# Performance work log

Hardware: AMD Instinct MI355X
Metric: run time of the kernel (lower is better)

The kernel has to match this reference:

```python
import jax, jax.numpy as jnp
import numpy as np

D_IN = 1024
D_OUT = 1024
NUM_HEADS = 16
HEAD_DIM = D_OUT // NUM_HEADS


def setup_inputs() -> dict:
    key = jax.random.key(0)
    ks = jax.random.split(key, 6)
    scale = 0.02
    x = jax.random.normal(ks[0], (4, 2048, D_IN), dtype=jnp.float32)
    Wq = jax.random.normal(ks[1], (D_IN, D_OUT), dtype=jnp.float32) * scale
    Wk = jax.random.normal(ks[2], (D_IN, D_OUT), dtype=jnp.float32) * scale
    Wv = jax.random.normal(ks[3], (D_IN, D_OUT), dtype=jnp.float32) * scale
    Wo = jax.random.normal(ks[4], (D_OUT, D_OUT), dtype=jnp.float32) * scale
    bo = jax.random.normal(ks[5], (D_OUT,), dtype=jnp.float32) * scale
    return {"x": x, "Wq": Wq, "Wk": Wk, "Wv": Wv, "Wo": Wo, "bo": bo}


def reference(x, Wq, Wk, Wv, Wo, bo):
    b, n, _ = x.shape
    # QKV projections -> [b, h, n, hd]
    def split_heads(t):
        return t.reshape(b, n, NUM_HEADS, HEAD_DIM).transpose(0, 2, 1, 3)
    q = split_heads(x @ Wq)
    k = split_heads(x @ Wk)
    v = split_heads(x @ Wv)
    # scaled causal attention scores [b, h, n, n]
    scores = jnp.einsum('bhqd,bhkd->bhqk', q, k) / jnp.sqrt(jnp.float32(HEAD_DIM))
    causal = jnp.tril(jnp.ones((n, n), dtype=bool))
    scores = jnp.where(causal, scores, -jnp.inf)
    attn = jax.nn.softmax(scores, axis=-1)
    # dropout p=0.0 -> identity
    ctx = jnp.einsum('bhqk,bhkd->bhqd', attn, v)  # [b, h, n, hd]
    ctx = ctx.transpose(0, 2, 1, 3).reshape(b, n, D_OUT)
    return ctx @ Wo + bo
```

## Files before the change

kernel.cpp:

```cpp
#include <hip/hip_runtime.h>
#include <hip/hip_bf16.h>

typedef __bf16 bf16;
typedef __attribute__((ext_vector_type(8))) __bf16 bf16x8;
typedef __attribute__((ext_vector_type(4))) __bf16 bf16x4;
typedef __attribute__((ext_vector_type(4))) float floatx4;

#define DM 1024
#define NH 16
#define HD 64
#define SEQ 2048
#define BATCH 4
#define MTOT (BATCH * SEQ)

#define GLDS(g, l) \
  __builtin_amdgcn_global_load_lds((const __attribute__((address_space(1))) void*)(g), \
                                   (__attribute__((address_space(3))) void*)(l), 16, 0, 0)

__global__ void cvt_f32_bf16(const float* __restrict__ in, bf16* __restrict__ out, int n4) {
  int i = blockIdx.x * 256 + threadIdx.x;
  if (i < n4) {
    float4 v = ((const float4*)in)[i];
    bf16x4 o;
    o[0] = (bf16)v.x; o[1] = (bf16)v.y; o[2] = (bf16)v.z; o[3] = (bf16)v.w;
    ((bf16x4*)out)[i] = o;
  }
}

__global__ void transpose_cvt4(const float* __restrict__ Wq, const float* __restrict__ Wk,
                               const float* __restrict__ Wv, const float* __restrict__ Wo,
                               bf16* __restrict__ Wqkvt, bf16* __restrict__ Wot) {
  __shared__ float tile[32][33];
  const float* W;
  bf16* Wt;
  int z = blockIdx.z;
  if (z == 0) { W = Wq; Wt = Wqkvt; }
  else if (z == 1) { W = Wk; Wt = Wqkvt + (size_t)DM * DM; }
  else if (z == 2) { W = Wv; Wt = Wqkvt + (size_t)2 * DM * DM; }
  else { W = Wo; Wt = Wot; }
  int n0 = blockIdx.x * 32, k0 = blockIdx.y * 32;
  int tx = threadIdx.x, ty = threadIdx.y;
#pragma unroll
  for (int j = 0; j < 32; j += 8)
    tile[ty + j][tx] = W[(size_t)(k0 + ty + j) * DM + n0 + tx];
  __syncthreads();
#pragma unroll
  for (int j = 0; j < 32; j += 8)
    Wt[(size_t)(n0 + ty + j) * DM + k0 + tx] = (bf16)tile[tx][ty + j];
}

#define BK 64

__global__ __launch_bounds__(256, 3) void gemm_qkv(const bf16* __restrict__ A,
                                                   const bf16* __restrict__ Bt,
                                                   bf16* __restrict__ Qb,
                                                   bf16* __restrict__ Kb,
                                                   bf16* __restrict__ Vt) {
  __shared__ __align__(16) bf16 Alds[128 * BK];
  __shared__ __align__(16) bf16 Blds[128 * BK];
  const int K = 1024;
  int m0 = blockIdx.x * 128;
  int n0 = blockIdx.y * 128;
  int tid = threadIdx.x;
  int wave = tid >> 6, lane = tid & 63;
  int wm = (wave & 1) * 64, wn = (wave >> 1) * 64;
  int lm = lane & 15, quad = lane >> 4;
  int lm7 = lm & 7;

  int cbase = wave * 64 + lane;
  const bf16* gA[4];
  const bf16* gB[4];
  bf16 *lA[4], *lB[4];
#pragma unroll
  for (int seg = 0; seg < 4; ++seg) {
    int c = seg * 256 + cbase;
    int row = c >> 3;
    int col8 = (c & 7) ^ (row & 7);
    gA[seg] = A + (size_t)(m0 + row) * K + col8 * 8;
    gB[seg] = Bt + (size_t)(n0 + row) * K + col8 * 8;
    lA[seg] = Alds + c * 8;
    lB[seg] = Blds + c * 8;
  }

  floatx4 acc[4][4] = {};
  for (int kt = 0; kt < K; kt += BK) {
    __syncthreads();
#pragma unroll
    for (int seg = 0; seg < 4; ++seg) {
      GLDS(gA[seg] + kt, lA[seg]);
      GLDS(gB[seg] + kt, lB[seg]);
    }
    __syncthreads();
#pragma unroll
    for (int ks = 0; ks < 2; ++ks) {
      int xk = (ks * 4 + quad) ^ lm7;
      bf16x8 af[4], bfr[4];
#pragma unroll
      for (int t = 0; t < 4; ++t) {
        af[t] = *(const bf16x8*)(Alds + (wm + t * 16 + lm) * BK + xk * 8);
        bfr[t] = *(const bf16x8*)(Blds + (wn + t * 16 + lm) * BK + xk * 8);
      }
#pragma unroll
      for (int i = 0; i < 4; ++i)
#pragma unroll
        for (int j = 0; j < 4; ++j)
          acc[i][j] = __builtin_amdgcn_mfma_f32_16x16x32_bf16(af[i], bfr[j], acc[i][j], 0, 0, 0);
    }
  }
#pragma unroll
  for (int i = 0; i < 4; ++i) {
#pragma unroll
    for (int j = 0; j < 4; ++j) {
#pragma unroll
      for (int r = 0; r < 4; ++r) {
        int R = m0 + wm + i * 16 + quad * 4 + r;
        int C = n0 + wn + j * 16 + lm;
        int b = R >> 11, n = R & 2047;
        int proj = C >> 10, c = C & 1023;
        int h = c >> 6, d = c & 63;
        int bh = b * NH + h;
        bf16 bv = (bf16)acc[i][j][r];
        if (proj == 0)
          Qb[((size_t)bh * SEQ + n) * HD + d] = bv;
        else if (proj == 1)
          Kb[((size_t)bh * SEQ + n) * HD + d] = bv;
        else
          Vt[((size_t)bh * HD + d) * SEQ + n] = bv;
      }
    }
  }
}

__global__ __launch_bounds__(256, 3) void gemm_out(const bf16* __restrict__ A,
                                                   const bf16* __restrict__ Bt,
                                                   const float* __restrict__ bias,
                                                   float* __restrict__ out) {
  __shared__ __align__(16) bf16 Alds[128 * BK];
  __shared__ __align__(16) bf16 Blds[128 * BK];
  const int K = 1024;
  int m0 = blockIdx.x * 128;
  int n0 = blockIdx.y * 128;
  int tid = threadIdx.x;
  int wave = tid >> 6, lane = tid & 63;
  int wm = (wave & 1) * 64, wn = (wave >> 1) * 64;
  int lm = lane & 15, quad = lane >> 4;
  int lm7 = lm & 7;

  int cbase = wave * 64 + lane;
  const bf16* gA[4];
  const bf16* gB[4];
  bf16 *lA[4], *lB[4];
#pragma unroll
  for (int seg = 0; seg < 4; ++seg) {
    int c = seg * 256 + cbase;
    int row = c >> 3;
    int col8 = (c & 7) ^ (row & 7);
    gA[seg] = A + (size_t)(m0 + row) * K + col8 * 8;
    gB[seg] = Bt + (size_t)(n0 + row) * K + col8 * 8;
    lA[seg] = Alds + c * 8;
    lB[seg] = Blds + c * 8;
  }

  floatx4 acc[4][4] = {};
  for (int kt = 0; kt < K; kt += BK) {
    __syncthreads();
#pragma unroll
    for (int seg = 0; seg < 4; ++seg) {
      GLDS(gA[seg] + kt, lA[seg]);
      GLDS(gB[seg] + kt, lB[seg]);
    }
    __syncthreads();
#pragma unroll
    for (int ks = 0; ks < 2; ++ks) {
      int xk = (ks * 4 + quad) ^ lm7;
      bf16x8 af[4], bfr[4];
#pragma unroll
      for (int t = 0; t < 4; ++t) {
        af[t] = *(const bf16x8*)(Alds + (wm + t * 16 + lm) * BK + xk * 8);
        bfr[t] = *(const bf16x8*)(Blds + (wn + t * 16 + lm) * BK + xk * 8);
      }
#pragma unroll
      for (int i = 0; i < 4; ++i)
#pragma unroll
        for (int j = 0; j < 4; ++j)
          acc[i][j] = __builtin_amdgcn_mfma_f32_16x16x32_bf16(af[i], bfr[j], acc[i][j], 0, 0, 0);
    }
  }
#pragma unroll
  for (int i = 0; i < 4; ++i)
#pragma unroll
    for (int j = 0; j < 4; ++j)
#pragma unroll
      for (int r = 0; r < 4; ++r) {
        int R = m0 + wm + i * 16 + quad * 4 + r;
        int C = n0 + wn + j * 16 + lm;
        out[(size_t)R * DM + C] = acc[i][j][r] + bias[C];
      }
}

#define SKV 72

__global__ __launch_bounds__(256) void attn(const bf16* __restrict__ Qb,
                                            const bf16* __restrict__ Kb,
                                            const bf16* __restrict__ Vt,
                                            bf16* __restrict__ ctx) {
  __shared__ __align__(16) bf16 Klds[64 * SKV];
  __shared__ __align__(16) bf16 Vlds[64 * SKV];
  int blk = blockIdx.x;
  int xcd = blk & 7;
  int idx = blk >> 3;
  int bh = (idx & 7) * 8 + xcd;
  int qt = 15 - (idx >> 3);
  int tid = threadIdx.x, wave = tid >> 6, lane = tid & 63;
  int lm = lane & 15, quad = lane >> 4;
  const bf16* Qp = Qb + (size_t)bh * SEQ * HD;
  const bf16* Kp = Kb + (size_t)bh * SEQ * HD;
  const bf16* Vp = Vt + (size_t)bh * HD * SEQ;
  int sr = tid >> 3, sc = (tid & 7) * 8;
  int b = bh >> 4, h = bh & 15;
  const float QSCALE = 0.125f * 1.4426950408889634f;

  bf16x8 ones;
#pragma unroll
  for (int j = 0; j < 8; ++j) ones[j] = (lm == 0) ? (bf16)1.0f : (bf16)0.0f;

  int q0 = qt * 128;
  int rowbase = q0 + wave * 32;

  bf16x8 qfA[2], qfB[2];
#pragma unroll
  for (int ks2 = 0; ks2 < 2; ++ks2) {
    bf16x8 qa = *(const bf16x8*)(Qp + (size_t)(rowbase + lm) * HD + ks2 * 32 + quad * 8);
    bf16x8 qb = *(const bf16x8*)(Qp + (size_t)(rowbase + 16 + lm) * HD + ks2 * 32 + quad * 8);
#pragma unroll
    for (int j = 0; j < 8; ++j) {
      qa[j] = (bf16)((float)qa[j] * QSCALE);
      qb[j] = (bf16)((float)qb[j] * QSCALE);
    }
    qfA[ks2] = qa;
    qfB[ks2] = qb;
  }

  floatx4 accA[4] = {}, accB[4] = {};
  floatx4 aclA = {}, aclB = {};
  int nkv = 2 * qt + 2;

  bf16x8 ka0 = *(const bf16x8*)(Kp + (size_t)sr * HD + sc);
  bf16x8 ka1 = *(const bf16x8*)(Kp + (size_t)(32 + sr) * HD + sc);
  bf16x8 va0 = *(const bf16x8*)(Vp + (size_t)sr * SEQ + sc);
  bf16x8 va1 = *(const bf16x8*)(Vp + (size_t)(32 + sr) * SEQ + sc);
  *(bf16x8*)(Klds + sr * SKV + sc) = ka0;
  *(bf16x8*)(Klds + (32 + sr) * SKV + sc) = ka1;
  *(bf16x8*)(Vlds + sr * SKV + sc) = va0;
  *(bf16x8*)(Vlds + (32 + sr) * SKV + sc) = va1;

#pragma unroll 1
  for (int t = 0; t < nkv; ++t) {
    __syncthreads();
    int kv0 = t * 64;
    if (t + 1 < nkv) {
      int kn = kv0 + 64;
      ka0 = *(const bf16x8*)(Kp + (size_t)(kn + sr) * HD + sc);
      ka1 = *(const bf16x8*)(Kp + (size_t)(kn + 32 + sr) * HD + sc);
      va0 = *(const bf16x8*)(Vp + (size_t)sr * SEQ + kn + sc);
      va1 = *(const bf16x8*)(Vp + (size_t)(32 + sr) * SEQ + kn + sc);
    }

    if (kv0 <= rowbase + 31) {
      floatx4 stA[4] = {}, stB[4] = {};
      __builtin_amdgcn_s_setprio(1);
#pragma unroll
      for (int mt = 0; mt < 4; ++mt) {
        bf16x8 kf0 = *(const bf16x8*)(Klds + (mt * 16 + lm) * SKV + quad * 8);
        bf16x8 kf1 = *(const bf16x8*)(Klds + (mt * 16 + lm) * SKV + 32 + quad * 8);
        stA[mt] = __builtin_amdgcn_mfma_f32_16x16x32_bf16(kf0, qfA[0], stA[mt], 0, 0, 0);
        stA[mt] = __builtin_amdgcn_mfma_f32_16x16x32_bf16(kf1, qfA[1], stA[mt], 0, 0, 0);
        stB[mt] = __builtin_amdgcn_mfma_f32_16x16x32_bf16(kf0, qfB[0], stB[mt], 0, 0, 0);
        stB[mt] = __builtin_amdgcn_mfma_f32_16x16x32_bf16(kf1, qfB[1], stB[mt], 0, 0, 0);
      }
      __builtin_amdgcn_s_setprio(0);

      bf16x4 pbA[4], pbB[4];
      if (kv0 + 63 <= rowbase) {
#pragma unroll
        for (int mt = 0; mt < 4; ++mt)
#pragma unroll
          for (int r = 0; r < 4; ++r) {
            pbA[mt][r] = (bf16)exp2f(stA[mt][r]);
            pbB[mt][r] = (bf16)exp2f(stB[mt][r]);
          }
      } else {
        int qrelA = rowbase - kv0 + lm;
        int qrelB = qrelA + 16;
#pragma unroll
        for (int mt = 0; mt < 4; ++mt)
#pragma unroll
          for (int r = 0; r < 4; ++r) {
            int kvrel = mt * 16 + quad * 4 + r;
            float pa = exp2f(stA[mt][r]);
            float pbv = exp2f(stB[mt][r]);
            if (kvrel > qrelA) pa = 0.f;
            if (kvrel > qrelB) pbv = 0.f;
            pbA[mt][r] = (bf16)pa;
            pbB[mt][r] = (bf16)pbv;
          }
      }

      __builtin_amdgcn_s_setprio(1);
#pragma unroll
      for (int ks = 0; ks < 2; ++ks) {
        bf16x8 pfA, pfB;
#pragma unroll
        for (int j = 0; j < 4; ++j) {
          pfA[j] = pbA[2 * ks][j]; pfA[4 + j] = pbA[2 * ks + 1][j];
          pfB[j] = pbB[2 * ks][j]; pfB[4 + j] = pbB[2 * ks + 1][j];
        }
        aclA = __builtin_amdgcn_mfma_f32_16x16x32_bf16(ones, pfA, aclA, 0, 0, 0);
        aclB = __builtin_amdgcn_mfma_f32_16x16x32_bf16(ones, pfB, aclB, 0, 0, 0);
#pragma unroll
        for (int db = 0; db < 4; ++db) {
          const bf16* vrow = Vlds + (db * 16 + lm) * SKV + ks * 32 + quad * 4;
          bf16x4 v0 = *(const bf16x4*)(vrow);
          bf16x4 v1 = *(const bf16x4*)(vrow + 16);
          bf16x8 vf;
#pragma unroll
          for (int j = 0; j < 4; ++j) { vf[j] = v0[j]; vf[4 + j] = v1[j]; }
          accA[db] = __builtin_amdgcn_mfma_f32_16x16x32_bf16(vf, pfA, accA[db], 0, 0, 0);
          accB[db] = __builtin_amdgcn_mfma_f32_16x16x32_bf16(vf, pfB, accB[db], 0, 0, 0);
        }
      }
      __builtin_amdgcn_s_setprio(0);
    }

    if (t + 1 < nkv) {
      __syncthreads();
      *(bf16x8*)(Klds + sr * SKV + sc) = ka0;
      *(bf16x8*)(Klds + (32 + sr) * SKV + sc) = ka1;
      *(bf16x8*)(Vlds + sr * SKV + sc) = va0;
      *(bf16x8*)(Vlds + (32 + sr) * SKV + sc) = va1;
    }
  }

  float linvA = 1.0f / __shfl(aclA[0], lm, 64);
  float linvB = 1.0f / __shfl(aclB[0], lm, 64);

  bf16* crowA = ctx + ((size_t)b * SEQ + rowbase + lm) * DM + h * 64;
  bf16* crowB = crowA + (size_t)16 * DM;
#pragma unroll
  for (int db = 0; db < 4; ++db) {
    bf16x4 oa, ob;
#pragma unroll
    for (int r = 0; r < 4; ++r) {
      oa[r] = (bf16)(accA[db][r] * linvA);
      ob[r] = (bf16)(accB[db][r] * linvB);
    }
    *(bf16x4*)(crowA + db * 16 + quad * 4) = oa;
    *(bf16x4*)(crowB + db * 16 + quad * 4) = ob;
  }
}

extern "C" void kernel_launch(void* const* d_in, const int* in_sizes, int n_in,
                              void* d_out, int out_size, void* d_ws, size_t ws_size,
                              hipStream_t stream) {
  const float* x = (const float*)d_in[0];
  const float* Wq = (const float*)d_in[1];
  const float* Wk = (const float*)d_in[2];
  const float* Wv = (const float*)d_in[3];
  const float* Wo = (const float*)d_in[4];
  const float* bo = (const float*)d_in[5];
  float* out = (float*)d_out;

  bf16* ws = (bf16*)d_ws;
  bf16* xb = ws;
  bf16* Wqkvt = xb + (size_t)MTOT * DM;
  bf16* Wot = Wqkvt + (size_t)3 * DM * DM;
  bf16* Qb = Wot + (size_t)DM * DM;
  bf16* Kb = Qb + (size_t)BATCH * NH * SEQ * HD;
  bf16* Vtb = Kb + (size_t)BATCH * NH * SEQ * HD;
  bf16* ctx = xb;

  cvt_f32_bf16<<<(MTOT * DM / 4 + 255) / 256, 256, 0, stream>>>(x, xb, MTOT * DM / 4);
  transpose_cvt4<<<dim3(32, 32, 4), dim3(32, 8), 0, stream>>>(Wq, Wk, Wv, Wo, Wqkvt, Wot);
  gemm_qkv<<<dim3(MTOT / 128, 3 * DM / 128), 256, 0, stream>>>(xb, Wqkvt, Qb, Kb, Vtb);
  attn<<<1024, 256, 0, stream>>>(Qb, Kb, Vtb, ctx);
  gemm_out<<<dim3(MTOT / 128, DM / 128), 256, 0, stream>>>(ctx, Wot, bo, out);
}
```

Before: 259.7 us.

## Pair causal query tiles per block and XOR-swizzle K/V shared memory

Each attention block now handles two query tiles (qt = 15-pr and pr), so every block does the same total causal work, and the grid drops from 1024 to 512 blocks. The padded LDS rows (stride 72) are replaced by unpadded 64-wide rows with an XOR swizzle. The V tile is also stored pre-interleaved, so each MFMA operand is one 16-byte LDS read instead of two 8-byte reads plus a repack. The setprio hints are removed. The aim is to remove tail imbalance and reduce LDS bank conflicts and read instructions, at the cost of fewer blocks to hide latency and a serial dependence between the two halves.

```diff
diff --git a/kernel.cpp b/kernel.cpp
--- a/kernel.cpp
+++ b/kernel.cpp
@@ -198,164 +198,172 @@
       }
 }
 
-#define SKV 72
-
 __global__ __launch_bounds__(256) void attn(const bf16* __restrict__ Qb,
                                             const bf16* __restrict__ Kb,
                                             const bf16* __restrict__ Vt,
                                             bf16* __restrict__ ctx) {
-  __shared__ __align__(16) bf16 Klds[64 * SKV];
-  __shared__ __align__(16) bf16 Vlds[64 * SKV];
+  __shared__ __align__(16) bf16 Klds[64 * 64];
+  __shared__ __align__(16) bf16 Vlds[64 * 64];
   int blk = blockIdx.x;
   int xcd = blk & 7;
   int idx = blk >> 3;
   int bh = (idx & 7) * 8 + xcd;
-  int qt = 15 - (idx >> 3);
+  int pr = idx >> 3;
   int tid = threadIdx.x, wave = tid >> 6, lane = tid & 63;
   int lm = lane & 15, quad = lane >> 4;
+  int lm7 = lm & 7;
   const bf16* Qp = Qb + (size_t)bh * SEQ * HD;
   const bf16* Kp = Kb + (size_t)bh * SEQ * HD;
   const bf16* Vp = Vt + (size_t)bh * HD * SEQ;
-  int sr = tid >> 3, sc = (tid & 7) * 8;
   int b = bh >> 4, h = bh & 15;
   const float QSCALE = 0.125f * 1.4426950408889634f;
 
+  int c1 = tid, c2 = tid + 256;
+  int r1 = c1 >> 3, l1 = (c1 & 7) ^ (r1 & 7);
+  int r2 = c2 >> 3, l2 = (c2 & 7) ^ (r2 & 7);
+  const bf16* Kg1 = Kp + (size_t)r1 * HD + l1 * 8;
+  const bf16* Kg2 = Kp + (size_t)r2 * HD + l2 * 8;
+  const bf16* Vg1 = Vp + (size_t)r1 * SEQ + (l1 >> 2) * 32 + (l1 & 3) * 4;
+  const bf16* Vg2 = Vp + (size_t)r2 * SEQ + (l2 >> 2) * 32 + (l2 & 3) * 4;
+
   bf16x8 ones;
 #pragma unroll
   for (int j = 0; j < 8; ++j) ones[j] = (lm == 0) ? (bf16)1.0f : (bf16)0.0f;
 
-  int q0 = qt * 128;
-  int rowbase = q0 + wave * 32;
-
-  bf16x8 qfA[2], qfB[2];
-#pragma unroll
-  for (int ks2 = 0; ks2 < 2; ++ks2) {
-    bf16x8 qa = *(const bf16x8*)(Qp + (size_t)(rowbase + lm) * HD + ks2 * 32 + quad * 8);
-    bf16x8 qb = *(const bf16x8*)(Qp + (size_t)(rowbase + 16 + lm) * HD + ks2 * 32 + quad * 8);
-#pragma unroll
-    for (int j = 0; j < 8; ++j) {
-      qa[j] = (bf16)((float)qa[j] * QSCALE);
-      qb[j] = (bf16)((float)qb[j] * QSCALE);
-    }
-    qfA[ks2] = qa;
-    qfB[ks2] = qb;
-  }
-
-  floatx4 accA[4] = {}, accB[4] = {};
-  floatx4 aclA = {}, aclB = {};
-  int nkv = 2 * qt + 2;
-
-  bf16x8 ka0 = *(const bf16x8*)(Kp + (size_t)sr * HD + sc);
-  bf16x8 ka1 = *(const bf16x8*)(Kp + (size_t)(32 + sr) * HD + sc);
-  bf16x8 va0 = *(const bf16x8*)(Vp + (size_t)sr * SEQ + sc);
-  bf16x8 va1 = *(const bf16x8*)(Vp + (size_t)(32 + sr) * SEQ + sc);
-  *(bf16x8*)(Klds + sr * SKV + sc) = ka0;
-  *(bf16x8*)(Klds + (32 + sr) * SKV + sc) = ka1;
-  *(bf16x8*)(Vlds + sr * SKV + sc) = va0;
-  *(bf16x8*)(Vlds + (32 + sr) * SKV + sc) = va1;
+  int xk0 = (quad ^ lm7) * 8;
+  int xk1 = ((4 + quad) ^ lm7) * 8;
 
 #pragma unroll 1
-  for (int t = 0; t < nkv; ++t) {
-    __syncthreads();
-    int kv0 = t * 64;
-    if (t + 1 < nkv) {
-      int kn = kv0 + 64;
-      ka0 = *(const bf16x8*)(Kp + (size_t)(kn + sr) * HD + sc);
-      ka1 = *(const bf16x8*)(Kp + (size_t)(kn + 32 + sr) * HD + sc);
-      va0 = *(const bf16x8*)(Vp + (size_t)sr * SEQ + kn + sc);
-      va1 = *(const bf16x8*)(Vp + (size_t)(32 + sr) * SEQ + kn + sc);
-    }
-
-    if (kv0 <= rowbase + 31) {
-      floatx4 stA[4] = {}, stB[4] = {};
-      __builtin_amdgcn_s_setprio(1);
-#pragma unroll
-      for (int mt = 0; mt < 4; ++mt) {
-        bf16x8 kf0 = *(const bf16x8*)(Klds + (mt * 16 + lm) * SKV + quad * 8);
-        bf16x8 kf1 = *(const bf16x8*)(Klds + (mt * 16 + lm) * SKV + 32 + quad * 8);
-        stA[mt] = __builtin_amdgcn_mfma_f32_16x16x32_bf16(kf0, qfA[0], stA[mt], 0, 0, 0);
-        stA[mt] = __builtin_amdgcn_mfma_f32_16x16x32_bf16(kf1, qfA[1], stA[mt], 0, 0, 0);
-        stB[mt] = __builtin_amdgcn_mfma_f32_16x16x32_bf16(kf0, qfB[0], stB[mt], 0, 0, 0);
-        stB[mt] = __builtin_amdgcn_mfma_f32_16x16x32_bf16(kf1, qfB[1], stB[mt], 0, 0, 0);
-      }
-      __builtin_amdgcn_s_setprio(0);
-
-      bf16x4 pbA[4], pbB[4];
-      if (kv0 + 63 <= rowbase) {
-#pragma unroll
-        for (int mt = 0; mt < 4; ++mt)
-#pragma unroll
-          for (int r = 0; r < 4; ++r) {
-            pbA[mt][r] = (bf16)exp2f(stA[mt][r]);
-            pbB[mt][r] = (bf16)exp2f(stB[mt][r]);
+  for (int half = 0; half < 2; ++half) {
+    int qt = half ? pr : 15 - pr;
+    int q0 = qt * 128;
+    int rowbase = q0 + wave * 32;
+    int nkv = 2 * qt + 2;
+
+    bf16x8 qfA[2], qfB[2];
+#pragma unroll
+    for (int ks2 = 0; ks2 < 2; ++ks2) {
+      bf16x8 qa = *(const bf16x8*)(Qp + (size_t)(rowbase + lm) * HD + ks2 * 32 + quad * 8);
+      bf16x8 qb = *(const bf16x8*)(Qp + (size_t)(rowbase + 16 + lm) * HD + ks2 * 32 + quad * 8);
+#pragma unroll
+      for (int j = 0; j < 8; ++j) {
+        qa[j] = (bf16)((float)qa[j] * QSCALE);
+        qb[j] = (bf16)((float)qb[j] * QSCALE);
+      }
+      qfA[ks2] = qa;
+      qfB[ks2] = qb;
+    }
+
+    floatx4 accA[4] = {}, accB[4] = {};
+    floatx4 aclA = {}, aclB = {};
+
+    if (half) __syncthreads();
+
+    bf16x8 k1 = *(const bf16x8*)Kg1;
+    bf16x8 k2 = *(const bf16x8*)Kg2;
+    bf16x4 v1a = *(const bf16x4*)Vg1, v1b = *(const bf16x4*)(Vg1 + 16);
+    bf16x4 v2a = *(const bf16x4*)Vg2, v2b = *(const bf16x4*)(Vg2 + 16);
+    *(bf16x8*)(Klds + c1 * 8) = k1;
+    *(bf16x8*)(Klds + c2 * 8) = k2;
+    *(bf16x4*)(Vlds + c1 * 8) = v1a;
+    *(bf16x4*)(Vlds + c1 * 8 + 4) = v1b;
+    *(bf16x4*)(Vlds + c2 * 8) = v2a;
+    *(bf16x4*)(Vlds + c2 * 8 + 4) = v2b;
+
+#pragma unroll 1
+    for (int t = 0; t < nkv; ++t) {
+      __syncthreads();
+      int kv0 = t * 64;
+      if (t + 1 < nkv) {
+        int kn = kv0 + 64;
+        k1 = *(const bf16x8*)(Kg1 + (size_t)kn * HD);
+        k2 = *(const bf16x8*)(Kg2 + (size_t)kn * HD);
+        v1a = *(const bf16x4*)(Vg1 + kn);
+        v1b = *(const bf16x4*)(Vg1 + kn + 16);
+        v2a = *(const bf16x4*)(Vg2 + kn);
+        v2b = *(const bf16x4*)(Vg2 + kn + 16);
+      }
+
+      if (kv0 <= rowbase + 31) {
+        floatx4 stA[4] = {}, stB[4] = {};
+#pragma unroll
+        for (int mt = 0; mt < 4; ++mt) {
+          const bf16* kr = Klds + (mt * 16 + lm) * 64;
+          bf16x8 kf0 = *(const bf16x8*)(kr + xk0);
+          bf16x8 kf1 = *(const bf16x8*)(kr + xk1);
+          stA[mt] = __builtin_amdgcn_mfma_f32_16x16x32_bf16(kf0, qfA[0], stA[mt], 0, 0, 0);
+          stA[mt] = __builtin_amdgcn_mfma_f32_16x16x32_bf16(kf1, qfA[1], stA[mt], 0, 0, 0);
+          stB[mt] = __builtin_amdgcn_mfma_f32_16x16x32_bf16(kf0, qfB[0], stB[mt], 0, 0, 0);
+          stB[mt] = __builtin_amdgcn_mfma_f32_16x16x32_bf16(kf1, qfB[1], stB[mt], 0, 0, 0);
+        }
+
+        bf16x8 pfA2[2], pfB2[2];
+        if (kv0 + 63 <= rowbase) {
+#pragma unroll
+          for (int mt = 0; mt < 4; ++mt)
+#pragma unroll
+            for (int r = 0; r < 4; ++r) {
+              pfA2[mt >> 1][(mt & 1) * 4 + r] = (bf16)exp2f(stA[mt][r]);
+              pfB2[mt >> 1][(mt & 1) * 4 + r] = (bf16)exp2f(stB[mt][r]);
+            }
+        } else {
+          int qrelA = rowbase - kv0 + lm;
+          int qrelB = qrelA + 16;
+#pragma unroll
+          for (int mt = 0; mt < 4; ++mt)
+#pragma unroll
+            for (int r = 0; r < 4; ++r) {
+              int kvrel = mt * 16 + quad * 4 + r;
+              float pa = exp2f(stA[mt][r]);
+              float pbv = exp2f(stB[mt][r]);
+              if (kvrel > qrelA) pa = 0.f;
+              if (kvrel > qrelB) pbv = 0.f;
+              pfA2[mt >> 1][(mt & 1) * 4 + r] = (bf16)pa;
+              pfB2[mt >> 1][(mt & 1) * 4 + r] = (bf16)pbv;
+            }
+        }
+
+#pragma unroll
+        for (int ks = 0; ks < 2; ++ks) {
+          int xv = ks ? xk1 : xk0;
+          aclA = __builtin_amdgcn_mfma_f32_16x16x32_bf16(ones, pfA2[ks], aclA, 0, 0, 0);
+          aclB = __builtin_amdgcn_mfma_f32_16x16x32_bf16(ones, pfB2[ks], aclB, 0, 0, 0);
+#pragma unroll
+          for (int db = 0; db < 4; ++db) {
+            bf16x8 vf = *(const bf16x8*)(Vlds + (db * 16 + lm) * 64 + xv);
+            accA[db] = __builtin_amdgcn_mfma_f32_16x16x32_bf16(vf, pfA2[ks], accA[db], 0, 0, 0);
+            accB[db] = __builtin_amdgcn_mfma_f32_16x16x32_bf16(vf, pfB2[ks], accB[db], 0, 0, 0);
           }
-      } else {
-        int qrelA = rowbase - kv0 + lm;
-        int qrelB = qrelA + 16;
-#pragma unroll
-        for (int mt = 0; mt < 4; ++mt)
-#pragma unroll
-          for (int r = 0; r < 4; ++r) {
-            int kvrel = mt * 16 + quad * 4 + r;
-            float pa = exp2f(stA[mt][r]);
-            float pbv = exp2f(stB[mt][r]);
-            if (kvrel > qrelA) pa = 0.f;
-            if (kvrel > qrelB) pbv = 0.f;
-            pbA[mt][r] = (bf16)pa;
-            pbB[mt][r] = (bf16)pbv;
-          }
-      }
-
-      __builtin_amdgcn_s_setprio(1);
-#pragma unroll
-      for (int ks = 0; ks < 2; ++ks) {
-        bf16x8 pfA, pfB;
-#pragma unroll
-        for (int j = 0; j < 4; ++j) {
-          pfA[j] = pbA[2 * ks][j]; pfA[4 + j] = pbA[2 * ks + 1][j];
-          pfB[j] = pbB[2 * ks][j]; pfB[4 + j] = pbB[2 * ks + 1][j];
         }
-        aclA = __builtin_amdgcn_mfma_f32_16x16x32_bf16(ones, pfA, aclA, 0, 0, 0);
-        aclB = __builtin_amdgcn_mfma_f32_16x16x32_bf16(ones, pfB, aclB, 0, 0, 0);
-#pragma unroll
-        for (int db = 0; db < 4; ++db) {
-          const bf16* vrow = Vlds + (db * 16 + lm) * SKV + ks * 32 + quad * 4;
-          bf16x4 v0 = *(const bf16x4*)(vrow);
-          bf16x4 v1 = *(const bf16x4*)(vrow + 16);
-          bf16x8 vf;
-#pragma unroll
-          for (int j = 0; j < 4; ++j) { vf[j] = v0[j]; vf[4 + j] = v1[j]; }
-          accA[db] = __builtin_amdgcn_mfma_f32_16x16x32_bf16(vf, pfA, accA[db], 0, 0, 0);
-          accB[db] = __builtin_amdgcn_mfma_f32_16x16x32_bf16(vf, pfB, accB[db], 0, 0, 0);
-        }
-      }
-      __builtin_amdgcn_s_setprio(0);
-    }
-
-    if (t + 1 < nkv) {
-      __syncthreads();
-      *(bf16x8*)(Klds + sr * SKV + sc) = ka0;
-      *(bf16x8*)(Klds + (32 + sr) * SKV + sc) = ka1;
-      *(bf16x8*)(Vlds + sr * SKV + sc) = va0;
-      *(bf16x8*)(Vlds + (32 + sr) * SKV + sc) = va1;
-    }
-  }
-
-  float linvA = 1.0f / __shfl(aclA[0], lm, 64);
-  float linvB = 1.0f / __shfl(aclB[0], lm, 64);
-
-  bf16* crowA = ctx + ((size_t)b * SEQ + rowbase + lm) * DM + h * 64;
-  bf16* crowB = crowA + (size_t)16 * DM;
-#pragma unroll
-  for (int db = 0; db < 4; ++db) {
-    bf16x4 oa, ob;
-#pragma unroll
-    for (int r = 0; r < 4; ++r) {
-      oa[r] = (bf16)(accA[db][r] * linvA);
-      ob[r] = (bf16)(accB[db][r] * linvB);
-    }
-    *(bf16x4*)(crowA + db * 16 + quad * 4) = oa;
-    *(bf16x4*)(crowB + db * 16 + quad * 4) = ob;
+      }
+
+      if (t + 1 < nkv) {
+        __syncthreads();
+        *(bf16x8*)(Klds + c1 * 8) = k1;
+        *(bf16x8*)(Klds + c2 * 8) = k2;
+        *(bf16x4*)(Vlds + c1 * 8) = v1a;
+        *(bf16x4*)(Vlds + c1 * 8 + 4) = v1b;
+        *(bf16x4*)(Vlds + c2 * 8) = v2a;
+        *(bf16x4*)(Vlds + c2 * 8 + 4) = v2b;
+      }
+    }
+
+    float linvA = 1.0f / __shfl(aclA[0], lm, 64);
+    float linvB = 1.0f / __shfl(aclB[0], lm, 64);
+
+    bf16* crowA = ctx + ((size_t)b * SEQ + rowbase + lm) * DM + h * 64;
+    bf16* crowB = crowA + (size_t)16 * DM;
+#pragma unroll
+    for (int db = 0; db < 4; ++db) {
+      bf16x4 oa, ob;
+#pragma unroll
+      for (int r = 0; r < 4; ++r) {
+        oa[r] = (bf16)(accA[db][r] * linvA);
+        ob[r] = (bf16)(accB[db][r] * linvB);
+      }
+      *(bf16x4*)(crowA + db * 16 + quad * 4) = oa;
+      *(bf16x4*)(crowB + db * 16 + quad * 4) = ob;
+    }
   }
 }
 
@@ -382,6 +390,6 @@
   cvt_f32_bf16<<<(MTOT * DM / 4 + 255) / 256, 256, 0, stream>>>(x, xb, MTOT * DM / 4);
   transpose_cvt4<<<dim3(32, 32, 4), dim3(32, 8), 0, stream>>>(Wq, Wk, Wv, Wo, Wqkvt, Wot);
   gemm_qkv<<<dim3(MTOT / 128, 3 * DM / 128), 256, 0, stream>>>(xb, Wqkvt, Qb, Kb, Vtb);
-  attn<<<1024, 256, 0, stream>>>(Qb, Kb, Vtb, ctx);
+  attn<<<512, 256, 0, stream>>>(Qb, Kb, Vtb, ctx);
   gemm_out<<<dim3(MTOT / 128, DM / 128), 256, 0, stream>>>(ctx, Wot, bo, out);
 }
```

Result: no change. 257.6 us (-0.8%).
